# Performance work log

Measured on AMD Instinct MI355X. Metric: run time of the kernel, lower is better.

Reference implementation:

```python
import jax, jax.numpy as jnp
import numpy as np
from jax import lax

INPUT_SIZE = 64          # classifier ROI size (init kwarg)
IMG = 640                # source image H=W
PROV, ALPHA, AD = 38, 25, 35
CONF_THRES, IOU_THRES = 0.25, 0.45
MAX_DET = 300            # yolov5 NMS max detections
FLAT = 16 * (INPUT_SIZE // 2) ** 2  # 16384


def setup_inputs() -> dict:
    key = jax.random.key(0)
    ks = jax.random.split(key, 12)
    B, N = 1, 25200
    xy = jax.random.uniform(ks[0], (B, N, 2), minval=32.0, maxval=608.0)
    wh = jax.random.uniform(ks[1], (B, N, 2), minval=16.0, maxval=128.0)
    obj = jax.random.uniform(ks[2], (B, N, 1))
    cls = jax.random.uniform(ks[3], (B, N, 1))
    preds = jnp.concatenate([xy, wh, obj, cls], axis=-1)  # [1,N,6] xywh+obj+cls
    image = jax.random.normal(ks[4], (B, 3, IMG, IMG), dtype=jnp.float32)
    W_conv = 0.1 * jax.random.normal(ks[5], (16, 3, 3, 3), dtype=jnp.float32)
    b_conv = jnp.zeros((16,), jnp.float32)
    W1 = 0.01 * jax.random.normal(ks[6], (8, FLAT, 128), dtype=jnp.float32)
    b1 = jnp.zeros((8, 128), jnp.float32)
    W2p = 0.05 * jax.random.normal(ks[7], (128, PROV), dtype=jnp.float32)
    b2p = jnp.zeros((PROV,), jnp.float32)
    W2a = 0.05 * jax.random.normal(ks[8], (128, ALPHA), dtype=jnp.float32)
    b2a = jnp.zeros((ALPHA,), jnp.float32)
    W2d = 0.05 * jax.random.normal(ks[9], (6, 128, AD), dtype=jnp.float32)
    b2d = jnp.zeros((6, AD), jnp.float32)
    return {"preds": preds, "image": image, "W_conv": W_conv, "b_conv": b_conv,
            "W1": W1, "b1": b1, "W2p": W2p, "b2p": b2p, "W2a": W2a, "b2a": b2a,
            "W2d": W2d, "b2d": b2d}


def _pairwise_iou(b):
    # b: [K,4] xyxy
    x1, y1, x2, y2 = b[:, 0], b[:, 1], b[:, 2], b[:, 3]
    area = (x2 - x1) * (y2 - y1)
    iw = jnp.clip(jnp.minimum(x2[:, None], x2[None, :]) - jnp.maximum(x1[:, None], x1[None, :]), 0.0)
    ih = jnp.clip(jnp.minimum(y2[:, None], y2[None, :]) - jnp.maximum(y1[:, None], y1[None, :]), 0.0)
    inter = iw * ih
    return inter / (area[:, None] + area[None, :] - inter + 1e-7)


def reference(preds, image, W_conv, b_conv, W1, b1, W2p, b2p, W2a, b2a, W2d, b2d):
    # ---- NMS (yolov5-style, single class) ----
    p = preds[0]                                   # [N,6]
    score = p[:, 4] * p[:, 5]                      # obj_conf * cls_conf
    xy, wh = p[:, 0:2], p[:, 2:4]
    boxes = jnp.concatenate([xy - wh / 2, xy + wh / 2], axis=-1)  # xyxy
    masked = jnp.where(score > CONF_THRES, score, -jnp.inf)
    top_s, idx = lax.top_k(masked, MAX_DET)        # sorted desc
    b = boxes[idx]                                 # [K,4]
    valid = top_s > CONF_THRES
    ious = _pairwise_iou(b)                        # [K,K]
    ar = jnp.arange(MAX_DET)

    def body(i, keep):
        sup = jnp.any((ious[i] > IOU_THRES) & keep & (ar < i))
        return keep.at[i].set(keep[i] & jnp.logical_not(sup))

    keep = lax.fori_loop(0, MAX_DET, body, valid)  # greedy suppression

    # ---- fixed-size ROI crop at box top-left (clipped) ----
    x1 = jnp.clip(jnp.round(b[:, 0]).astype(jnp.int32), 0, IMG - INPUT_SIZE)
    y1 = jnp.clip(jnp.round(b[:, 1]).astype(jnp.int32), 0, IMG - INPUT_SIZE)
    img0 = image[0]                                # [3,H,W]
    crops = jax.vmap(lambda y, x: lax.dynamic_slice(img0, (0, y, x), (3, INPUT_SIZE, INPUT_SIZE)))(y1, x1)

    # ---- LicensePlateClassifier: conv->relu->maxpool->flatten->8 heads ----
    conv = lax.conv_general_dilated(crops, W_conv, (1, 1), 'SAME',
                                    dimension_numbers=('NCHW', 'OIHW', 'NCHW'))
    conv = jax.nn.relu(conv + b_conv[None, :, None, None])
    pooled = lax.reduce_window(conv, -jnp.inf, lax.max, (1, 1, 2, 2), (1, 1, 2, 2), 'VALID')
    feats = pooled.reshape(MAX_DET, FLAT)          # NCHW flatten == torch.flatten(x,1)
    h = jax.nn.relu(jnp.einsum('kf,hfd->hkd', feats, W1) + b1[:, None, :])  # [8,K,128]
    out_p = h[0] @ W2p + b2p                       # [K,38]
    out_a = h[1] @ W2a + b2a                       # [K,25]
    out_d = jnp.einsum('hkd,hdo->hko', h[2:], W2d) + b2d[:, None, :]        # [6,K,35]
    out_d = out_d.transpose(1, 0, 2).reshape(MAX_DET, 6 * AD)
    logits = jnp.concatenate([out_p, out_a, out_d], axis=1)  # [K,273]
    return logits * keep.astype(logits.dtype)[:, None]
```

## Files before the change

kernel.cpp:

```cpp
#include <hip/hip_runtime.h>

#define N_PRED 25200
#define CONF 0.25f
#define IOU_THR 0.45f
#define MAXD 300
#define IMGW 640
#define CROPW 64
#define HISTN 16640

typedef float f32x4 __attribute__((ext_vector_type(4)));
typedef short s16x8 __attribute__((ext_vector_type(8)));
typedef unsigned long long u64;

#define OFF_HIST   0u
#define OFF_CNT    66560u
#define OFF_CUT    66624u
#define OFF_CAND   66816u
#define CTRL_BYTES 75008u
#define OFF_BOXES  75008u
#define OFF_XY1    79872u
#define OFF_VALID  82432u
#define OFF_KEEP   83712u
#define OFF_SUP    84992u
#define OFF_H      97024u
#define OFF_FEATS  1325824u
#define OFF_PART   11811584u

__device__ inline unsigned short f2bf(float x) {
  unsigned u = __float_as_uint(x);
  u += 0x7FFFu + ((u >> 16) & 1u);
  return (unsigned short)(u >> 16);
}

__device__ inline void gload_lds16(const void* g, void* l) {
  __builtin_amdgcn_global_load_lds(
      (const __attribute__((address_space(1))) void*)g,
      (__attribute__((address_space(3))) void*)l, 16, 0, 0);
}

__global__ __launch_bounds__(256) void k_hist(const float* __restrict__ preds,
                                              unsigned* __restrict__ hist) {
  int i = blockIdx.x * 256 + threadIdx.x;
  if (i >= N_PRED) return;
  float s = preds[i * 6 + 4] * preds[i * 6 + 5];
  if (s > CONF) atomicAdd(&hist[__float_as_uint(s) >> 16], 1u);
}

__global__ __launch_bounds__(256) void k_findcut(const unsigned* __restrict__ hist,
                                                 unsigned* __restrict__ cut) {
  __shared__ unsigned s[256];
  int t = threadIdx.x;
  int base = t * 65;
  unsigned local = 0;
  for (int i = 0; i < 65; ++i) local += hist[base + i];
  s[t] = local;
  __syncthreads();
  for (int off = 1; off < 256; off <<= 1) {
    unsigned add = (t + off < 256) ? s[t + off] : 0u;
    __syncthreads();
    s[t] += add;
    __syncthreads();
  }
  unsigned incl = s[t];
  unsigned excl = (t < 255) ? s[t + 1] : 0u;
  if (incl >= (unsigned)MAXD && excl < (unsigned)MAXD) {
    unsigned acc = excl, res = 0u;
    #pragma unroll
    for (int ii = 64; ii >= 0; --ii) {
      acc += hist[base + ii];
      if (res == 0u && acc >= (unsigned)MAXD) res = (unsigned)(base + ii);
    }
    cut[0] = res;
  }
}

__global__ __launch_bounds__(256) void k_compact(const float* __restrict__ preds,
                                                 const unsigned* __restrict__ cut,
                                                 unsigned* __restrict__ cnt,
                                                 u64* __restrict__ cand) {
  int i = blockIdx.x * 256 + threadIdx.x;
  if (i >= N_PRED) return;
  float s = preds[i * 6 + 4] * preds[i * 6 + 5];
  if (s <= CONF) return;
  unsigned bits = __float_as_uint(s);
  if ((bits >> 16) < cut[0]) return;
  unsigned pos = atomicAdd(cnt, 1u);
  if (pos < 1024u)
    cand[pos] = ((u64)bits << 32) | (u64)(0xFFFFFFFFu - (unsigned)i);
}

__global__ __launch_bounds__(1024) void k_sortprep(const float* __restrict__ preds,
                                                   const u64* __restrict__ cand,
                                                   float* __restrict__ boxes,
                                                   int* __restrict__ xy1,
                                                   float* __restrict__ validf) {
  __shared__ u64 sk[1024];
  int t = threadIdx.x;
  sk[t] = cand[t];
  __syncthreads();
  for (int k = 2; k <= 1024; k <<= 1)
    for (int j = k >> 1; j > 0; j >>= 1) {
      int p = t ^ j;
      if (p > t) {
        u64 a = sk[t], b = sk[p];
        bool up = ((t & k) == 0);
        bool sw = up ? (a < b) : (a > b);
        if (sw) { sk[t] = b; sk[p] = a; }
      }
      __syncthreads();
    }
  if (t < MAXD) {
    u64 key = sk[t];
    if (key != 0ull) {
      int idx = (int)(0xFFFFFFFFu - (unsigned)(key & 0xFFFFFFFFull));
      float cx = preds[idx * 6 + 0], cy = preds[idx * 6 + 1];
      float w  = preds[idx * 6 + 2], h  = preds[idx * 6 + 3];
      float x1 = cx - w * 0.5f, y1 = cy - h * 0.5f;
      float x2 = cx + w * 0.5f, y2 = cy + h * 0.5f;
      boxes[t * 4 + 0] = x1; boxes[t * 4 + 1] = y1;
      boxes[t * 4 + 2] = x2; boxes[t * 4 + 3] = y2;
      int xi = (int)rintf(x1); xi = min(max(xi, 0), IMGW - CROPW);
      int yi = (int)rintf(y1); yi = min(max(yi, 0), IMGW - CROPW);
      xy1[t * 2 + 0] = xi; xy1[t * 2 + 1] = yi;
      validf[t] = 1.0f;
    } else {
      boxes[t * 4 + 0] = 0.f; boxes[t * 4 + 1] = 0.f;
      boxes[t * 4 + 2] = 0.f; boxes[t * 4 + 3] = 0.f;
      xy1[t * 2 + 0] = 0; xy1[t * 2 + 1] = 0;
      validf[t] = 0.f;
    }
  }
}

__global__ __launch_bounds__(320) void k_iou(const float* __restrict__ boxes,
                                             u64* __restrict__ sup) {
  int i = blockIdx.x, t = threadIdx.x;
  int w = t >> 6, lane = t & 63;
  f32x4 bi = *(const f32x4*)&boxes[i * 4];
  f32x4 bj = (t < MAXD) ? *(const f32x4*)&boxes[t * 4]
                        : (f32x4){0.f, 0.f, 0.f, 0.f};
  float ar  = (bi[2] - bi[0]) * (bi[3] - bi[1]);
  float arj = (bj[2] - bj[0]) * (bj[3] - bj[1]);
  float iw = fmaxf(fminf(bi[2], bj[2]) - fmaxf(bi[0], bj[0]), 0.f);
  float ih = fmaxf(fminf(bi[3], bj[3]) - fmaxf(bi[1], bj[1]), 0.f);
  float inter = iw * ih;
  float iou = inter / (ar + arj - inter + 1e-7f);
  u64 bm = __ballot((t < MAXD) && (iou > IOU_THR));
  if (lane == 0) sup[i * 5 + w] = bm;
}

__global__ __launch_bounds__(64) void k_nms(const u64* __restrict__ sup,
                                            const float* __restrict__ validf,
                                            float* __restrict__ keepf) {
  int lane = threadIdx.x;
  u64 srow[5][5];
  #pragma unroll
  for (int c = 0; c < 5; ++c)
    #pragma unroll
    for (int ww = 0; ww < 5; ++ww) srow[c][ww] = 0ull;
  #pragma unroll
  for (int c = 0; c < 5; ++c) {
    int i = c * 64 + lane;
    if (i < MAXD) {
      #pragma unroll
      for (int ww = 0; ww <= c; ++ww) srow[c][ww] = sup[i * 5 + ww];
    }
  }
  u64 validm[5];
  #pragma unroll
  for (int c = 0; c < 5; ++c) {
    int i = c * 64 + lane;
    float vf = (i < MAXD) ? validf[i] : 0.f;
    validm[c] = __ballot(vf > 0.5f);
  }
  u64 kw0 = 0, kw1 = 0, kw2 = 0, kw3 = 0;
  #pragma unroll
  for (int c = 0; c < 5; ++c) {
    bool ext = ((srow[c][0] & kw0) | (srow[c][1] & kw1) |
                (srow[c][2] & kw2) | (srow[c][3] & kw3)) != 0ull;
    u64 alive = validm[c] & __ballot(!ext);
    unsigned mlo = (unsigned)srow[c][c], mhi = (unsigned)(srow[c][c] >> 32);
    u64 rem = alive;
    while (rem) {
      int b = (int)__builtin_ctzll(rem);
      u64 gt = (b == 63) ? 0ull : (~0ull << (b + 1));
      u64 mi = ((u64)(unsigned)__builtin_amdgcn_readlane((int)mhi, b) << 32) |
               (u64)(unsigned)__builtin_amdgcn_readlane((int)mlo, b);
      alive &= ~(mi & gt);
      rem = alive & gt;
    }
    int i = c * 64 + lane;
    if (i < MAXD) keepf[i] = ((alive >> lane) & 1ull) ? 1.f : 0.f;
    if (c == 0) kw0 = alive;
    else if (c == 1) kw1 = alive;
    else if (c == 2) kw2 = alive;
    else if (c == 3) kw3 = alive;
  }
}

__global__ __launch_bounds__(256) void k_cropconv(const float* __restrict__ image,
                                                  const float* __restrict__ Wc,
                                                  const float* __restrict__ bc,
                                                  const int* __restrict__ xy1,
                                                  short* __restrict__ feats) {
  __shared__ __align__(16) float crop[3][10][68];
  int det = blockIdx.x, sl = blockIdx.y, tid = threadIdx.x;
  int pr0 = sl * 4;
  int gyBase = pr0 * 2 - 1;
  int ch = tid >> 4, px = tid & 15;

  float w[27];
  #pragma unroll
  for (int i = 0; i < 27; i++) w[i] = Wc[ch * 27 + i];
  float bias = bc[ch];

  int x0 = xy1[det * 2 + 0], y0 = xy1[det * 2 + 1];
  float sv[8];
  #pragma unroll
  for (int i = 0; i < 8; i++) {
    int u = tid + i * 256;
    float v = 0.f;
    if (u < 1920) {
      int row = u >> 6, x = u & 63;
      int c = row / 10, ry = row - c * 10;
      int gy = gyBase + ry;
      if (gy >= 0 && gy < CROPW)
        v = image[(size_t)c * (IMGW * IMGW) + (y0 + gy) * IMGW + x0 + x];
    }
    sv[i] = v;
  }
  if (tid < 120) {
    int row = tid >> 2, e = tid & 3;
    int c = row / 10, ry = row - c * 10;
    crop[c][ry][(e == 0) ? 0 : (64 + e)] = 0.f;
  }
  #pragma unroll
  for (int i = 0; i < 8; i++) {
    int u = tid + i * 256;
    if (u < 1920) {
      int row = u >> 6, x = u & 63;
      int c = row / 10, ry = row - c * 10;
      crop[c][ry][x + 1] = sv[i];
    }
  }
  __syncthreads();
  #pragma unroll
  for (int pr = 0; pr < 4; pr++) {
    float acc0[4] = {0.f, 0.f, 0.f, 0.f};
    float acc1[4] = {0.f, 0.f, 0.f, 0.f};
    #pragma unroll
    for (int c = 0; c < 3; c++) {
      #pragma unroll
      for (int r = 0; r < 4; r++) {
        const float* rp = &crop[c][2 * pr + r][4 * px];
        f32x4 v4 = *(const f32x4*)rp;
        float2 v2 = *(const float2*)(rp + 4);
        float in[6] = {v4[0], v4[1], v4[2], v4[3], v2.x, v2.y};
        if (r <= 2) {
          const float w0 = w[c * 9 + r * 3], w1 = w[c * 9 + r * 3 + 1],
                      w2 = w[c * 9 + r * 3 + 2];
          #pragma unroll
          for (int q = 0; q < 4; q++)
            acc0[q] += in[q] * w0 + in[q + 1] * w1 + in[q + 2] * w2;
        }
        if (r >= 1) {
          const float w0 = w[c * 9 + (r - 1) * 3], w1 = w[c * 9 + (r - 1) * 3 + 1],
                      w2 = w[c * 9 + (r - 1) * 3 + 2];
          #pragma unroll
          for (int q = 0; q < 4; q++)
            acc1[q] += in[q] * w0 + in[q + 1] * w1 + in[q + 2] * w2;
        }
      }
    }
    float m0 = fmaxf(fmaxf(acc0[0], acc0[1]), fmaxf(acc1[0], acc1[1]));
    float m1 = fmaxf(fmaxf(acc0[2], acc0[3]), fmaxf(acc1[2], acc1[3]));
    unsigned lo = f2bf(fmaxf(m0 + bias, 0.f));
    unsigned hi = f2bf(fmaxf(m1 + bias, 0.f));
    *(unsigned*)&feats[(size_t)det * 16384 + ch * 1024 + (pr0 + pr) * 32 + 2 * px] =
        lo | (hi << 16);
  }
}

__global__ __launch_bounds__(512, 4) void k_gemm(const short* __restrict__ feats,
                                                 const float* __restrict__ W1,
                                                 float* __restrict__ part,
                                                 int ntiles) {
  __shared__ __align__(16) short As[320 * 64];
  int tid = threadIdx.x;
  int wid = tid >> 6, lane = tid & 63;
  int wm = wid & 3, wn = wid >> 2;
  int lr = lane & 15, kg = lane >> 4;
  int ks = blockIdx.x, hd = blockIdx.y, dh = blockIdx.z;
  const int f0 = ks * ntiles * 64, d0 = dh * 64;
  const float* w1h = W1 + (size_t)hd * 16384 * 128;

  int gm = wid * 40 + (lane >> 3);
  int gc = lane & 7;
  char* ldsbase = (char*)As + wid * 5120;

  f32x4 acc[5][2];
  #pragma unroll
  for (int i = 0; i < 5; i++)
    #pragma unroll
    for (int j = 0; j < 2; j++) acc[i][j] = (f32x4){0.f, 0.f, 0.f, 0.f};

  #pragma unroll
  for (int i = 0; i < 5; i++) {
    int m = gm + i * 8;
    gload_lds16(feats + (size_t)m * 16384 + f0 + ((gc ^ (m & 7)) << 3),
                ldsbase + i * 1024);
  }
  __syncthreads();

  const float* bp = w1h + (size_t)(f0 + kg * 8) * 128 + d0 + wn * 32 + lr;

  for (int t = 0; t < ntiles; ++t) {
    const float* bpt = bp + (size_t)t * 64 * 128;
    float bF[2][2][8];
    #pragma unroll
    for (int k32 = 0; k32 < 2; k32++)
      #pragma unroll
      for (int nf = 0; nf < 2; nf++)
        #pragma unroll
        for (int j = 0; j < 8; j++)
          bF[k32][nf][j] = bpt[(k32 * 32 + j) * 128 + nf * 16];
    #pragma unroll
    for (int k32 = 0; k32 < 2; ++k32) {
      s16x8 af[5];
      #pragma unroll
      for (int mf = 0; mf < 5; ++mf) {
        int row = wm * 80 + mf * 16 + lr;
        int c = k32 * 4 + kg;
        af[mf] = *(const s16x8*)((const char*)As + row * 128 + ((c ^ (row & 7)) << 4));
      }
      s16x8 bfr[2];
      #pragma unroll
      for (int nf = 0; nf < 2; nf++)
        #pragma unroll
        for (int j = 0; j < 8; j++)
          bfr[nf][j] = (short)f2bf(bF[k32][nf][j]);
      #pragma unroll
      for (int nf = 0; nf < 2; ++nf)
        #pragma unroll
        for (int mf = 0; mf < 5; ++mf)
          acc[mf][nf] = __builtin_amdgcn_mfma_f32_16x16x32_bf16(af[mf], bfr[nf], acc[mf][nf], 0, 0, 0);
    }
    if ((t + 1) < ntiles) {
      __syncthreads();
      int f1 = f0 + (t + 1) * 64;
      #pragma unroll
      for (int i = 0; i < 5; i++) {
        int m = gm + i * 8;
        gload_lds16(feats + (size_t)m * 16384 + f1 + ((gc ^ (m & 7)) << 3),
                    ldsbase + i * 1024);
      }
      __syncthreads();
    }
  }
  #pragma unroll
  for (int mf = 0; mf < 5; ++mf)
    #pragma unroll
    for (int nf = 0; nf < 2; ++nf)
      #pragma unroll
      for (int r = 0; r < 4; ++r) {
        int m = wm * 80 + mf * 16 + kg * 4 + r;
        int d = d0 + wn * 32 + nf * 16 + lr;
        part[(((size_t)ks * 8 + hd) * 320 + m) * 128 + d] = acc[mf][nf][r];
      }
}

__global__ __launch_bounds__(256) void k_reduce(const float* __restrict__ part,
                                                const float* __restrict__ b1,
                                                float* __restrict__ h,
                                                int nks) {
  int o = blockIdx.x * 256 + threadIdx.x;
  int d = o & 127;
  int k = (o >> 7) % 300;
  int hh = o / (128 * 300);
  float s = 0.f;
  for (int ksp = 0; ksp < nks; ksp++)
    s += part[(((size_t)ksp * 8 + hh) * 320 + k) * 128 + d];
  s += b1[hh * 128 + d];
  h[o] = fmaxf(s, 0.f);
}

__global__ __launch_bounds__(320) void k_fc2(const float* __restrict__ h,
                                             const float* __restrict__ keepf,
                                             const float* __restrict__ W2p,
                                             const float* __restrict__ b2p,
                                             const float* __restrict__ W2a,
                                             const float* __restrict__ b2a,
                                             const float* __restrict__ W2d,
                                             const float* __restrict__ b2d,
                                             float* __restrict__ out) {
  int det = blockIdx.x, t = threadIdx.x;
  __shared__ float hl[1024];
  for (int i = t; i < 1024; i += 320) {
    int hh = i >> 7, d = i & 127;
    hl[i] = h[((size_t)hh * 300 + det) * 128 + d];
  }
  __syncthreads();
  if (t >= 273) return;
  float kf = keepf[det];
  float s = 0.f, bias;
  if (t < 38) {
    const float* hp = hl;
    for (int d = 0; d < 128; d++) s += hp[d] * W2p[d * 38 + t];
    bias = b2p[t];
  } else if (t < 63) {
    int c = t - 38;
    const float* hp = hl + 128;
    for (int d = 0; d < 128; d++) s += hp[d] * W2a[d * 25 + c];
    bias = b2a[c];
  } else {
    int u = t - 63, j = u / 35, o = u - j * 35;
    const float* hp = hl + (2 + j) * 128;
    for (int d = 0; d < 128; d++) s += hp[d] * W2d[((size_t)j * 128 + d) * 35 + o];
    bias = b2d[j * 35 + o];
  }
  out[det * 273 + t] = (s + bias) * kf;
}

extern "C" void kernel_launch(void* const* d_in, const int* in_sizes, int n_in,
                              void* d_out, int out_size, void* d_ws, size_t ws_size,
                              hipStream_t stream) {
  (void)in_sizes; (void)n_in; (void)out_size;
  const float* preds = (const float*)d_in[0];
  const float* image = (const float*)d_in[1];
  const float* Wc    = (const float*)d_in[2];
  const float* bc    = (const float*)d_in[3];
  const float* W1    = (const float*)d_in[4];
  const float* b1    = (const float*)d_in[5];
  const float* W2p   = (const float*)d_in[6];
  const float* b2p   = (const float*)d_in[7];
  const float* W2a   = (const float*)d_in[8];
  const float* b2a   = (const float*)d_in[9];
  const float* W2d   = (const float*)d_in[10];
  const float* b2d   = (const float*)d_in[11];

  char* ws = (char*)d_ws;
  unsigned* hist   = (unsigned*)(ws + OFF_HIST);
  unsigned* cnt    = (unsigned*)(ws + OFF_CNT);
  unsigned* cut    = (unsigned*)(ws + OFF_CUT);
  u64*      cand   = (u64*)(ws + OFF_CAND);
  float*    boxes  = (float*)(ws + OFF_BOXES);
  int*      xy1    = (int*)(ws + OFF_XY1);
  float*    validf = (float*)(ws + OFF_VALID);
  float*    keepf  = (float*)(ws + OFF_KEEP);
  u64*      sup    = (u64*)(ws + OFF_SUP);
  float*    hbuf   = (float*)(ws + OFF_H);
  short*    feats  = (short*)(ws + OFF_FEATS);
  float*    part   = (float*)(ws + OFF_PART);
  float*    out    = (float*)d_out;

  int nks = (ws_size >= (size_t)OFF_PART + 32ull * 8 * 320 * 128 * 4) ? 32 : 16;
  int ntiles = 256 / nks;

  hipMemsetAsync(ws, 0, CTRL_BYTES, stream);
  k_hist<<<(N_PRED + 255) / 256, 256, 0, stream>>>(preds, hist);
  k_findcut<<<1, 256, 0, stream>>>(hist, cut);
  k_compact<<<(N_PRED + 255) / 256, 256, 0, stream>>>(preds, cut, cnt, cand);
  k_sortprep<<<1, 1024, 0, stream>>>(preds, cand, boxes, xy1, validf);
  k_iou<<<MAXD, 320, 0, stream>>>(boxes, sup);
  k_nms<<<1, 64, 0, stream>>>(sup, validf, keepf);
  k_cropconv<<<dim3(300, 8), 256, 0, stream>>>(image, Wc, bc, xy1, feats);
  k_gemm<<<dim3(nks, 8, 2), 512, 0, stream>>>(feats, W1, part, ntiles);
  k_reduce<<<1200, 256, 0, stream>>>(part, b1, hbuf, nks);
  k_fc2<<<MAXD, 320, 0, stream>>>(hbuf, keepf, W2p, b2p, W2a, b2a, W2d, b2d, out);
}
```

Before: 132.6 us.

## Double-buffer GEMM tiles in LDS and stage W1 through shared memory

The bf16 MFMA GEMM kernel now splits the M dimension across blocks, doubling the grid. It double-buffers both the feature tile and the fp32 W1 tile in LDS with async global-to-LDS loads, so the next tile is fetched while the current one is computed. This replaces the per-thread scattered global reads of W1 into registers with coalesced staged loads, and removes one barrier per iteration. The cost is that W1 is now read twice (once per M-half), LDS use is higher, and the B fragment is gathered from LDS with strided scalar reads.

```diff
diff --git a/kernel.cpp b/kernel.cpp
--- a/kernel.cpp
+++ b/kernel.cpp
@@ -285,45 +285,48 @@
                                                  const float* __restrict__ W1,
                                                  float* __restrict__ part,
                                                  int ntiles) {
-  __shared__ __align__(16) short As[320 * 64];
+  __shared__ __align__(16) short As[2][160 * 64];
+  __shared__ __align__(16) float Bs[2][64 * 64];
   int tid = threadIdx.x;
   int wid = tid >> 6, lane = tid & 63;
-  int wm = wid & 3, wn = wid >> 2;
+  int wm = wid & 1, wn = (wid >> 1) & 3;
   int lr = lane & 15, kg = lane >> 4;
-  int ks = blockIdx.x, hd = blockIdx.y, dh = blockIdx.z;
-  const int f0 = ks * ntiles * 64, d0 = dh * 64;
+  int ks = blockIdx.x, hd = blockIdx.y;
+  int md = blockIdx.z >> 1, dh = blockIdx.z & 1;
+  const int f0 = ks * ntiles * 64, d0 = dh * 64, m0 = md * 160;
   const float* w1h = W1 + (size_t)hd * 16384 * 128;
 
-  int gm = wid * 40 + (lane >> 3);
-  int gc = lane & 7;
-  char* ldsbase = (char*)As + wid * 5120;
-
-  f32x4 acc[5][2];
-  #pragma unroll
-  for (int i = 0; i < 5; i++)
-    #pragma unroll
-    for (int j = 0; j < 2; j++) acc[i][j] = (f32x4){0.f, 0.f, 0.f, 0.f};
-
-  #pragma unroll
-  for (int i = 0; i < 5; i++) {
-    int m = gm + i * 8;
-    gload_lds16(feats + (size_t)m * 16384 + f0 + ((gc ^ (m & 7)) << 3),
-                ldsbase + i * 1024);
-  }
+  f32x4 acc[5];
+  #pragma unroll
+  for (int i = 0; i < 5; i++) acc[i] = (f32x4){0.f, 0.f, 0.f, 0.f};
+
+  auto stage = [&](int t, int buf) {
+    int kt = f0 + t * 64;
+    if (wid < 4) {
+      #pragma unroll
+      for (int i = 0; i < 5; i++) {
+        int rbase = wid * 40 + i * 8;
+        int swz = (lane & 7) ^ (lane >> 3);
+        gload_lds16(feats + (size_t)(m0 + rbase + (lane >> 3)) * 16384 + kt + swz * 8,
+                    (char*)&As[buf][0] + rbase * 128);
+      }
+    } else {
+      int wb = wid - 4;
+      #pragma unroll
+      for (int i = 0; i < 4; i++) {
+        int krow = (wb * 4 + i) * 4 + (lane >> 4);
+        gload_lds16(w1h + (size_t)(kt + krow) * 128 + d0 + (lane & 15) * 4,
+                    (char*)&Bs[buf][0] + (wb * 4 + i) * 1024);
+      }
+    }
+  };
+
+  stage(0, 0);
   __syncthreads();
 
-  const float* bp = w1h + (size_t)(f0 + kg * 8) * 128 + d0 + wn * 32 + lr;
-
   for (int t = 0; t < ntiles; ++t) {
-    const float* bpt = bp + (size_t)t * 64 * 128;
-    float bF[2][2][8];
-    #pragma unroll
-    for (int k32 = 0; k32 < 2; k32++)
-      #pragma unroll
-      for (int nf = 0; nf < 2; nf++)
-        #pragma unroll
-        for (int j = 0; j < 8; j++)
-          bF[k32][nf][j] = bpt[(k32 * 32 + j) * 128 + nf * 16];
+    int cur = t & 1;
+    if (t + 1 < ntiles) stage(t + 1, cur ^ 1);
     #pragma unroll
     for (int k32 = 0; k32 < 2; ++k32) {
       s16x8 af[5];
@@ -331,42 +334,26 @@
       for (int mf = 0; mf < 5; ++mf) {
         int row = wm * 80 + mf * 16 + lr;
         int c = k32 * 4 + kg;
-        af[mf] = *(const s16x8*)((const char*)As + row * 128 + ((c ^ (row & 7)) << 4));
+        af[mf] = *(const s16x8*)((const char*)&As[cur][0] + row * 128 + ((c ^ (row & 7)) << 4));
       }
-      s16x8 bfr[2];
-      #pragma unroll
-      for (int nf = 0; nf < 2; nf++)
-        #pragma unroll
-        for (int j = 0; j < 8; j++)
-          bfr[nf][j] = (short)f2bf(bF[k32][nf][j]);
-      #pragma unroll
-      for (int nf = 0; nf < 2; ++nf)
-        #pragma unroll
-        for (int mf = 0; mf < 5; ++mf)
-          acc[mf][nf] = __builtin_amdgcn_mfma_f32_16x16x32_bf16(af[mf], bfr[nf], acc[mf][nf], 0, 0, 0);
-    }
-    if ((t + 1) < ntiles) {
-      __syncthreads();
-      int f1 = f0 + (t + 1) * 64;
-      #pragma unroll
-      for (int i = 0; i < 5; i++) {
-        int m = gm + i * 8;
-        gload_lds16(feats + (size_t)m * 16384 + f1 + ((gc ^ (m & 7)) << 3),
-                    ldsbase + i * 1024);
-      }
-      __syncthreads();
-    }
+      s16x8 bfr;
+      #pragma unroll
+      for (int j = 0; j < 8; j++)
+        bfr[j] = (short)f2bf(Bs[cur][(k32 * 32 + kg * 8 + j) * 64 + wn * 16 + lr]);
+      #pragma unroll
+      for (int mf = 0; mf < 5; ++mf)
+        acc[mf] = __builtin_amdgcn_mfma_f32_16x16x32_bf16(af[mf], bfr, acc[mf], 0, 0, 0);
+    }
+    __syncthreads();
   }
   #pragma unroll
   for (int mf = 0; mf < 5; ++mf)
     #pragma unroll
-    for (int nf = 0; nf < 2; ++nf)
-      #pragma unroll
-      for (int r = 0; r < 4; ++r) {
-        int m = wm * 80 + mf * 16 + kg * 4 + r;
-        int d = d0 + wn * 32 + nf * 16 + lr;
-        part[(((size_t)ks * 8 + hd) * 320 + m) * 128 + d] = acc[mf][nf][r];
-      }
+    for (int r = 0; r < 4; ++r) {
+      int m = m0 + wm * 80 + mf * 16 + kg * 4 + r;
+      int d = d0 + wn * 16 + lr;
+      part[(((size_t)ks * 8 + hd) * 320 + m) * 128 + d] = acc[mf][r];
+    }
 }
 
 __global__ __launch_bounds__(256) void k_reduce(const float* __restrict__ part,
@@ -464,7 +451,7 @@
   k_iou<<<MAXD, 320, 0, stream>>>(boxes, sup);
   k_nms<<<1, 64, 0, stream>>>(sup, validf, keepf);
   k_cropconv<<<dim3(300, 8), 256, 0, stream>>>(image, Wc, bc, xy1, feats);
-  k_gemm<<<dim3(nks, 8, 2), 512, 0, stream>>>(feats, W1, part, ntiles);
+  k_gemm<<<dim3(nks, 8, 4), 512, 0, stream>>>(feats, W1, part, ntiles);
   k_reduce<<<1200, 256, 0, stream>>>(part, b1, hbuf, nks);
   k_fc2<<<MAXD, 320, 0, stream>>>(hbuf, keepf, W2p, b2p, W2a, b2a, W2d, b2d, out);
 }
```

New measurement: 138.2 us. +4.2%, slower.
